# Optimization experiments

Hardware: AMD Instinct MI355X
Metric: run time of the kernel (lower is better)

Reference implementation:

```python
import jax, jax.numpy as jnp
import numpy as np

N, E, H, RBF, NZ = 15000, 300000, 128, 20, 119
CUTOFF, BOX = 6.0, 7.0


def setup_inputs() -> dict:
    key = jax.random.key(0)
    ks = jax.random.split(key, 24)
    s = 0.05

    def rn(k, shape):
        return jax.random.normal(k, shape, dtype=jnp.float32) * s

    z = jax.random.randint(ks[0], (N,), 0, 83)
    pos = jax.random.uniform(ks[1], (N, 3), dtype=jnp.float32) * BOX
    src = jax.random.randint(ks[2], (E,), 0, N)
    dst = (src + jax.random.randint(ks[3], (E,), 1, N)) % N  # guarantees src != dst
    edge_index = jnp.stack([src, dst], axis=0)  # (2, E)
    cell_offsets = (jax.random.randint(ks[4], (E, 3), 0, 3) - 1).astype(jnp.float32)
    cell = jnp.eye(3, dtype=jnp.float32) * BOX
    return dict(
        z=z, pos=pos, edge_index=edge_index, cell_offsets=cell_offsets, cell=cell,
        embed=rn(ks[5], (NZ, H)),
        msg_w1=rn(ks[6], (3, H, H)), msg_b1=rn(ks[7], (3, H)),
        msg_w2=rn(ks[8], (3, H, 3 * H)), msg_b2=rn(ks[9], (3, 3 * H)),
        filt_w=rn(ks[10], (3, RBF, 3 * H)), filt_b=rn(ks[11], (3, 3 * H)),
        upd_uw=rn(ks[12], (3, H, H)), upd_ub=rn(ks[13], (3, H)),
        upd_vw=rn(ks[14], (3, H, H)), upd_vb=rn(ks[15], (3, H)),
        upd_mw1=rn(ks[16], (3, 2 * H, H)), upd_mb1=rn(ks[17], (3, H)),
        upd_mw2=rn(ks[18], (3, H, 3 * H)), upd_mb2=rn(ks[19], (3, 3 * H)),
        head_w1=rn(ks[20], (H, H)), head_b1=rn(ks[21], (H,)),
        head_w2=rn(ks[22], (H, H)), head_b2=rn(ks[23], (H,)),
    )


def reference(z, pos, edge_index, cell_offsets, cell, embed,
              msg_w1, msg_b1, msg_w2, msg_b2, filt_w, filt_b,
              upd_uw, upd_ub, upd_vw, upd_vb,
              upd_mw1, upd_mb1, upd_mw2, upd_mb2,
              head_w1, head_b1, head_w2, head_b2):
    n_nodes = z.shape[0]
    hdim = embed.shape[1]
    row, col = edge_index[0], edge_index[1]  # receiver, sender (DeepDFT convention)

    # get_pbc_distances
    offsets = cell_offsets @ cell                                  # (E,3)
    edge_diff = pos[row] - pos[col] + offsets                      # (E,3)
    edge_dist = jnp.linalg.norm(edge_diff, axis=-1)                # (E,)
    unit = edge_diff / edge_dist[:, None]                          # (E,3)

    # sinc radial basis + cosine cutoff (shared by all message layers)
    n = jnp.arange(1, RBF + 1, dtype=pos.dtype)
    rbf = jnp.sin(edge_dist[:, None] * n * jnp.pi / CUTOFF) / edge_dist[:, None]  # (E,RBF)
    fcut = jnp.where(edge_dist < CUTOFF,
                     0.5 * (jnp.cos(jnp.pi * edge_dist / CUTOFF) + 1.0), 0.0)      # (E,)

    ns = embed[z]                                                  # (N,H)
    nv = jnp.zeros((n_nodes, 3, hdim), dtype=pos.dtype)            # (N,3,H)

    for i in range(3):
        # ---- PainnMessage ----
        filt = (rbf @ filt_w[i] + filt_b[i]) * fcut[:, None]       # (E,3H)
        sout = jax.nn.silu(ns @ msg_w1[i] + msg_b1[i]) @ msg_w2[i] + msg_b2[i]  # (N,3H)
        fo = filt * sout[col]                                      # (E,3H)
        gate_v, gate_e, msg_s = jnp.split(fo, 3, axis=1)           # each (E,H)
        msg_v = nv[col] * gate_v[:, None, :] + gate_e[:, None, :] * unit[:, :, None]  # (E,3,H)
        ns = ns + jax.ops.segment_sum(msg_s, row, num_segments=n_nodes)
        nv = nv + jax.ops.segment_sum(msg_v, row, num_segments=n_nodes)
        # ---- PainnUpdate ----
        Uv = nv @ upd_uw[i] + upd_ub[i]                            # (N,3,H)
        Vv = nv @ upd_vw[i] + upd_vb[i]                            # (N,3,H)
        mlp_in = jnp.concatenate([jnp.linalg.norm(Vv, axis=1), ns], axis=1)  # (N,2H)
        m = jax.nn.silu(mlp_in @ upd_mw1[i] + upd_mb1[i]) @ upd_mw2[i] + upd_mb2[i]  # (N,3H)
        a_vv, a_sv, a_ss = jnp.split(m, 3, axis=1)
        inner = jnp.sum(Uv * Vv, axis=1)                           # (N,H)
        nv = nv + a_vv[:, None, :] * Uv
        ns = ns + a_sv * inner + a_ss

    v = jax.nn.silu(ns @ head_w1 + head_b1) @ head_w2 + head_b2    # (N,H)
    return v, edge_dist
```

## Files before the change

### kernel.cpp

```cpp
#include <hip/hip_runtime.h>
#include <math.h>

#define HD 128
#define H3 384
#define RBF_N 20
#define CUTOFF_R 6.0f
#define PI_F 3.14159265358979323846f
#define CAPE 40000

#define PITCH 136

typedef __attribute__((ext_vector_type(8))) short short8v;
typedef __attribute__((ext_vector_type(4))) short short4v;
typedef __attribute__((ext_vector_type(4))) float f32x4;
typedef unsigned short bf_t;

__device__ __forceinline__ float silu_f(float x) { return x / (1.0f + __expf(-x)); }

__device__ __forceinline__ ushort f2bf(float f) {
    union { float f; uint u; } v; v.f = f;
    return (ushort)((v.u + 0x7FFF + ((v.u >> 16) & 1)) >> 16);
}
__device__ __forceinline__ float bf2f(ushort x) {
    union { uint u; float f; } v; v.u = ((uint)x) << 16;
    return v.f;
}

#define LOADWG(r, CNT, NTH, W, rowlen, koff)                                   \
    _Pragma("unroll")                                                          \
    for (int it_ = 0; it_ < CNT; ++it_) {                                      \
        int u_ = tid + it_ * NTH;                                              \
        (r)[it_] = *(const short8v*)((W) + (size_t)(u_ >> 4) * (rowlen) +      \
                                     (koff) + ((u_ & 15) << 3));               \
    }
#define COMMITB(r, CNT, NTH, WT)                                               \
    _Pragma("unroll")                                                          \
    for (int it_ = 0; it_ < CNT; ++it_) {                                      \
        int u_ = tid + it_ * NTH;                                              \
        *(short8v*)&WT[(u_ >> 4) * PITCH + ((u_ & 15) << 3)] = (r)[it_];       \
    }
#define MFMA8B(Abuf, acc, WT)                                                  \
    _Pragma("unroll")                                                          \
    for (int step_ = 0; step_ < 4; ++step_) {                                  \
        int kb_ = step_ * 32 + lk;                                             \
        short8v a_ = *(const short8v*)&(Abuf)[(wr + lr) * PITCH + kb_];        \
        (acc)[0] = __builtin_amdgcn_mfma_f32_16x16x32_bf16(                    \
            a_, *(const short8v*)&WT[(wn + lr) * PITCH + kb_], (acc)[0], 0, 0, 0); \
        (acc)[1] = __builtin_amdgcn_mfma_f32_16x16x32_bf16(                    \
            a_, *(const short8v*)&WT[(wn + 16 + lr) * PITCH + kb_], (acc)[1], 0, 0, 0); \
    }
#define MFMA8R(Abuf, acc)                                                      \
    _Pragma("unroll")                                                          \
    for (int step_ = 0; step_ < 4; ++step_) {                                  \
        int kb_ = step_ * 32 + lk;                                             \
        short8v a_ = *(const short8v*)&(Abuf)[(wr + lr) * PITCH + kb_];        \
        (acc)[0] = __builtin_amdgcn_mfma_f32_16x16x32_bf16(                    \
            a_, *(const short8v*)&Wt[(wn + lr) * PITCH + kb_], (acc)[0], 0, 0, 0); \
        (acc)[1] = __builtin_amdgcn_mfma_f32_16x16x32_bf16(                    \
            a_, *(const short8v*)&Wt[(wn + 16 + lr) * PITCH + kb_], (acc)[1], 0, 0, 0); \
    }
#define COMMITWG(r, CNT, NTH)                                                  \
    _Pragma("unroll")                                                          \
    for (int it_ = 0; it_ < CNT; ++it_) {                                      \
        int u_ = tid + it_ * NTH;                                              \
        *(short8v*)&Wt[(u_ >> 4) * PITCH + ((u_ & 15) << 3)] = (r)[it_];       \
    }

__device__ __forceinline__ void wcvt(const float* __restrict__ src, bf_t* __restrict__ dst,
                                     int idx, int K, int N) {
    int per = K * N;
    int l = idx / per, r = idx % per;
    int k = r / N, n = r % N;
    dst[(size_t)l*per + (size_t)n*K + k] = f2bf(src[(size_t)l*per + (size_t)k*N + n]);
}

__global__ void setup1_kernel(const float* __restrict__ pos, const int* __restrict__ ei,
                              const float* __restrict__ cofs, const float* __restrict__ cell,
                              float* __restrict__ dist_out, int* __restrict__ deg, int E, int eb,
                              const float* s0, const float* s1, const float* s2, const float* s3,
                              const float* s4, const float* s5, const float* s6, const float* s7,
                              const float* s8, bf_t* __restrict__ dst) {
    if ((int)blockIdx.x < eb) {
        int e = blockIdx.x * 256 + threadIdx.x;
        if (e >= E) return;
        int r = ei[e], c = ei[E + e];
        float c0 = cofs[3*e], c1 = cofs[3*e+1], c2 = cofs[3*e+2];
        float d0 = pos[3*r]   - pos[3*c]   + c0*cell[0] + c1*cell[3] + c2*cell[6];
        float d1 = pos[3*r+1] - pos[3*c+1] + c0*cell[1] + c1*cell[4] + c2*cell[7];
        float d2 = pos[3*r+2] - pos[3*c+2] + c0*cell[2] + c1*cell[5] + c2*cell[8];
        float dist = sqrtf(d0*d0 + d1*d1 + d2*d2);
        dist_out[e] = dist;
        if (dist < CUTOFF_R) atomicAdd(&deg[r], 1);
    } else {
        int i = (blockIdx.x - eb) * 256 + threadIdx.x;
        if (i < 49152)        wcvt(s0, dst + 0,      i - 0,      128, 128);
        else if (i < 196608)  wcvt(s1, dst + 49152,  i - 49152,  128, 384);
        else if (i < 245760)  wcvt(s2, dst + 196608, i - 196608, 128, 128);
        else if (i < 294912)  wcvt(s3, dst + 245760, i - 245760, 128, 128);
        else if (i < 393216)  wcvt(s4, dst + 294912, i - 294912, 256, 128);
        else if (i < 540672)  wcvt(s5, dst + 393216, i - 393216, 128, 384);
        else if (i < 557056)  wcvt(s6, dst + 540672, i - 540672, 128, 128);
        else if (i < 573440)  wcvt(s7, dst + 557056, i - 557056, 128, 128);
        else if (i < 596480)  dst[i] = f2bf(s8[i - 573440]);
    }
}

__global__ void scan_kernel(const int* __restrict__ deg, int* __restrict__ off,
                            int* __restrict__ cursor, int n) {
    __shared__ int wsum[16];
    __shared__ int carry_s;
    const int tid = threadIdx.x;
    const int lane = tid & 63, wv = tid >> 6;
    if (tid == 0) carry_s = 0;
    __syncthreads();
    for (int base = 0; base < n; base += 1024) {
        int v = (base + tid < n) ? deg[base + tid] : 0;
        int x = v;
        #pragma unroll
        for (int s = 1; s < 64; s <<= 1) {
            int y = __shfl_up(x, s);
            if (lane >= s) x += y;
        }
        if (lane == 63) wsum[wv] = x;
        __syncthreads();
        if (tid == 0) {
            int a = carry_s;
            #pragma unroll
            for (int i = 0; i < 16; ++i) { int t = wsum[i]; wsum[i] = a; a += t; }
            carry_s = a;
        }
        __syncthreads();
        int exc = wsum[wv] + x - v;
        if (base + tid < n) { off[base + tid] = exc; cursor[base + tid] = exc; }
        __syncthreads();
    }
    if (tid == 0) off[n] = carry_s;
}

__global__ __launch_bounds__(512) void setup2_kernel(
        const float* __restrict__ pos, const int* __restrict__ ei,
        const float* __restrict__ cofs, const float* __restrict__ cell,
        const float* __restrict__ dist_in, int* __restrict__ cursor,
        int* __restrict__ col_s, float* __restrict__ fcut_s,
        float* __restrict__ unit_s, float* __restrict__ rbf_s, int E, int sb,
        const int* __restrict__ z, const float* __restrict__ emb,
        bf_t* __restrict__ nsb,
        const bf_t* __restrict__ W1b, const float* __restrict__ b1,
        const bf_t* __restrict__ W2b, const float* __restrict__ b2,
        bf_t* __restrict__ Cb, int M) {
    __shared__ ushort As[32 * PITCH];
    __shared__ ushort Wt[128 * PITCH];
    __shared__ ushort Hid[32 * PITCH];
    const int tid = threadIdx.x;

    if ((int)blockIdx.x < sb) {
        int e = blockIdx.x * 512 + tid;
        if (e >= E) return;
        float dist = dist_in[e];
        if (!(dist < CUTOFF_R)) return;
        int r = ei[e], c = ei[E + e];
        float c0 = cofs[3*e], c1 = cofs[3*e+1], c2 = cofs[3*e+2];
        float d0 = pos[3*r]   - pos[3*c]   + c0*cell[0] + c1*cell[3] + c2*cell[6];
        float d1 = pos[3*r+1] - pos[3*c+1] + c0*cell[1] + c1*cell[4] + c2*cell[7];
        float d2 = pos[3*r+2] - pos[3*c+2] + c0*cell[2] + c1*cell[5] + c2*cell[8];
        int p = atomicAdd(&cursor[r], 1);
        if (p >= CAPE) return;
        col_s[p] = c;
        fcut_s[p] = 0.5f * (cosf(PI_F * dist / CUTOFF_R) + 1.0f);
        float inv = 1.0f / dist;
        unit_s[3*p]   = d0 * inv;
        unit_s[3*p+1] = d1 * inv;
        unit_s[3*p+2] = d2 * inv;
        #pragma unroll
        for (int j = 0; j < RBF_N; ++j)
            rbf_s[(size_t)p*RBF_N + j] = sinf(dist * (float)(j+1) * (PI_F / CUTOFF_R)) * inv;
        return;
    }

    const int m0 = (blockIdx.x - sb) * 32;
    const int wid = tid >> 6, lane = tid & 63;
    const int wr = (wid >> 2) * 16;
    const int wn = (wid & 3) * 32;
    const int lr = lane & 15, lk = (lane >> 4) << 3;
    const int er = (lane >> 4) << 2;

    short8v rwA[4], rwB[4];
    LOADWG(rwA, 4, 512, W1b, 128, 0);
    {
        int row = tid >> 4, k8 = (tid & 15) << 3;
        int m = m0 + row;
        short8v pk = (short8v)(0);
        if (m < M) {
            const float* ep = emb + (size_t)z[m] * HD + k8;
            const float4 x = *(const float4*)ep, y = *(const float4*)(ep + 4);
            pk[0]=(short)f2bf(x.x); pk[1]=(short)f2bf(x.y);
            pk[2]=(short)f2bf(x.z); pk[3]=(short)f2bf(x.w);
            pk[4]=(short)f2bf(y.x); pk[5]=(short)f2bf(y.y);
            pk[6]=(short)f2bf(y.z); pk[7]=(short)f2bf(y.w);
            *(short8v*)(nsb + (size_t)m * HD + k8) = pk;
        }
        *(short8v*)&As[row * PITCH + k8] = pk;
    }
    __syncthreads();
    COMMITWG(rwA, 4, 512); LOADWG(rwB, 4, 512, W2b, 128, 0);
    __syncthreads();
    f32x4 acc1[2];
    acc1[0] = (f32x4)(0.f); acc1[1] = (f32x4)(0.f);
    MFMA8R(As, acc1);
    __syncthreads();
    COMMITWG(rwB, 4, 512); LOADWG(rwA, 4, 512, W2b + 16384, 128, 0);
    #pragma unroll
    for (int j = 0; j < 2; ++j) {
        int col = wn + 16 * j + lr;
        float bb = b1[col];
        #pragma unroll
        for (int r = 0; r < 4; ++r)
            Hid[(wr + er + r) * PITCH + col] = f2bf(silu_f(acc1[j][r] + bb));
    }
    __syncthreads();
    {
        f32x4 a0[2]; a0[0] = (f32x4)(0.f); a0[1] = (f32x4)(0.f);
        MFMA8R(Hid, a0);
        __syncthreads();
        COMMITWG(rwA, 4, 512); LOADWG(rwB, 4, 512, W2b + 32768, 128, 0);
        #pragma unroll
        for (int j = 0; j < 2; ++j) {
            int col = wn + 16 * j + lr;
            float bb = b2[col];
            #pragma unroll
            for (int r = 0; r < 4; ++r) {
                int m = m0 + wr + er + r;
                if (m < M) Cb[(size_t)m * H3 + col] = f2bf(a0[j][r] + bb);
            }
        }
        __syncthreads();
    }
    {
        f32x4 a1[2]; a1[0] = (f32x4)(0.f); a1[1] = (f32x4)(0.f);
        MFMA8R(Hid, a1);
        __syncthreads();
        COMMITWG(rwB, 4, 512);
        #pragma unroll
        for (int j = 0; j < 2; ++j) {
            int col = wn + 16 * j + lr;
            float bb = b2[128 + col];
            #pragma unroll
            for (int r = 0; r < 4; ++r) {
                int m = m0 + wr + er + r;
                if (m < M) Cb[(size_t)m * H3 + 128 + col] = f2bf(a1[j][r] + bb);
            }
        }
        __syncthreads();
    }
    {
        f32x4 a2[2]; a2[0] = (f32x4)(0.f); a2[1] = (f32x4)(0.f);
        MFMA8R(Hid, a2);
        #pragma unroll
        for (int j = 0; j < 2; ++j) {
            int col = wn + 16 * j + lr;
            float bb = b2[256 + col];
            #pragma unroll
            for (int r = 0; r < 4; ++r) {
                int m = m0 + wr + er + r;
                if (m < M) Cb[(size_t)m * H3 + 256 + col] = f2bf(a2[j][r] + bb);
            }
        }
    }
}

template <int MODE>
__global__ __launch_bounds__(1024) void upd_fused(const bf_t* __restrict__ nv2p,
                                                 const bf_t* __restrict__ Ub,
                                                 const bf_t* __restrict__ Vb,
                                                 const float* __restrict__ bu,
                                                 const float* __restrict__ bv,
                                                 bf_t* __restrict__ nvp,
                                                 bf_t* __restrict__ nsb,
                                                 const bf_t* __restrict__ W1b,
                                                 const float* __restrict__ b1,
                                                 const bf_t* __restrict__ W2b,
                                                 const float* __restrict__ b2,
                                                 const bf_t* __restrict__ xw1,
                                                 const float* __restrict__ xb1,
                                                 const bf_t* __restrict__ xw2,
                                                 const float* __restrict__ xb2,
                                                 bf_t* __restrict__ soutb,
                                                 float* __restrict__ Cf,
                                                 int N) {
    __shared__ ushort As3[3][64 * PITCH];
    __shared__ ushort Wt0[128 * PITCH];
    __shared__ ushort Wt1[128 * PITCH];
    __shared__ ushort Hid[64 * PITCH];
    __shared__ ushort AsG[64 * PITCH];
    const int tid = threadIdx.x;
    const int m0 = blockIdx.x * 64;
    const int wid = tid >> 6, lane = tid & 63;
    const int wr = (wid >> 2) * 16;
    const int wn = (wid & 3) * 32;
    const int lr = lane & 15, lk = (lane >> 4) << 3;
    const int er = (lane >> 4) << 2;
    const size_t NHD = (size_t)N * HD;

    short8v rwA[2], rwB[2];
    LOADWG(rwA, 2, 1024, Ub, 128, 0);

    #pragma unroll
    for (int it = 0; it < 3; ++it) {
        int u = tid + it * 1024;
        int d = u >> 10, v = u & 1023;
        int row = v >> 4, k8 = (v & 15) << 3;
        int m = m0 + row;
        short8v pk = (short8v)(0);
        if (m < N) pk = *(const short8v*)(nv2p + (size_t)d * NHD + (size_t)m * HD + k8);
        *(short8v*)&As3[d][row * PITCH + k8] = pk;
    }
    {
        int row = tid >> 4, k8 = (tid & 15) << 3;
        int m = m0 + row;
        short8v pk = (short8v)(0);
        if (m < N) pk = *(const short8v*)(nsb + (size_t)m * HD + k8);
        *(short8v*)&AsG[row * PITCH + k8] = pk;
    }
    __syncthreads();
    COMMITB(rwA, 2, 1024, Wt0); LOADWG(rwB, 2, 1024, Vb, 128, 0);
    __syncthreads();

    f32x4 aU[3][2], aV[3][2];
    #pragma unroll
    for (int d = 0; d < 3; ++d) {
        aU[d][0] = (f32x4)(0.f); aU[d][1] = (f32x4)(0.f);
        aV[d][0] = (f32x4)(0.f); aV[d][1] = (f32x4)(0.f);
    }
    #pragma unroll
    for (int d = 0; d < 3; ++d) { MFMA8B(As3[d], aU[d], Wt0); }
    COMMITB(rwB, 2, 1024, Wt1); LOADWG(rwA, 2, 1024, W1b, 256, 0);
    __syncthreads();

    #pragma unroll
    for (int d = 0; d < 3; ++d) { MFMA8B(As3[d], aV[d], Wt1); }
    float inn_r[2][4];
    #pragma unroll
    for (int j = 0; j < 2; ++j) {
        int col = wn + 16 * j + lr;
        float bbu = bu[col], bbv = bv[col];
        #pragma unroll
        for (int r = 0; r < 4; ++r) {
            float inn = 0.f, nrm = 0.f;
            #pragma unroll
            for (int d = 0; d < 3; ++d) {
                float u = aU[d][j][r] + bbu;
                float v = aV[d][j][r] + bbv;
                aU[d][j][r] = u;
                inn += u * v;
                nrm += v * v;
            }
            inn_r[j][r] = inn;
            Hid[(wr + er + r) * PITCH + col] = f2bf(sqrtf(nrm));
        }
    }
    COMMITB(rwA, 2, 1024, Wt0); LOADWG(rwB, 2, 1024, W1b, 256, 128);
    __syncthreads();

    f32x4 acc1[2]; acc1[0] = (f32x4)(0.f); acc1[1] = (f32x4)(0.f);
    MFMA8B(Hid, acc1, Wt0);
    COMMITB(rwB, 2, 1024, Wt1);
    if (MODE == 1) { LOADWG(rwA, 2, 1024, W2b, 128, 0); }
    else           { LOADWG(rwA, 2, 1024, W2b + 16384, 128, 0); }
    __syncthreads();

    MFMA8B(AsG, acc1, Wt1);
    #pragma unroll
    for (int j = 0; j < 2; ++j) {
        int col = wn + 16 * j + lr;
        float bb = b1[col];
        #pragma unroll
        for (int r = 0; r < 4; ++r)
            Hid[(wr + er + r) * PITCH + col] = f2bf(silu_f(acc1[j][r] + bb));
    }
    COMMITB(rwA, 2, 1024, Wt0);
    if (MODE == 1) { LOADWG(rwB, 2, 1024, W2b + 16384, 128, 0); }
    else           { LOADWG(rwB, 2, 1024, W2b + 32768, 128, 0); }
    __syncthreads();

    float sv[2][4];
    if (MODE == 1) {
        f32x4 g0[2]; g0[0] = (f32x4)(0.f); g0[1] = (f32x4)(0.f);
        MFMA8B(Hid, g0, Wt0);
        #pragma unroll
        for (int j = 0; j < 2; ++j) {
            int col = wn + 16 * j + lr;
            float bb = b2[col];
            #pragma unroll
            for (int r = 0; r < 4; ++r) {
                int m = m0 + wr + er + r;
                if (m < N) {
                    float g = g0[j][r] + bb;
                    #pragma unroll
                    for (int d = 0; d < 3; ++d) {
                        float pp = bf2f(As3[d][(wr + er + r) * PITCH + col]);
                        nvp[(size_t)d * NHD + (size_t)m * HD + col] =
                            f2bf(pp + g * aU[d][j][r]);
                    }
                }
            }
        }
        COMMITB(rwB, 2, 1024, Wt1); LOADWG(rwA, 2, 1024, W2b + 32768, 128, 0);
        __syncthreads();
        f32x4 g1[2]; g1[0] = (f32x4)(0.f); g1[1] = (f32x4)(0.f);
        MFMA8B(Hid, g1, Wt1);
        #pragma unroll
        for (int j = 0; j < 2; ++j) {
            int col = wn + 16 * j + lr;
            float bb = b2[128 + col];
            #pragma unroll
            for (int r = 0; r < 4; ++r)
                sv[j][r] = (g1[j][r] + bb) * inn_r[j][r];
        }
        COMMITB(rwA, 2, 1024, Wt0); LOADWG(rwB, 2, 1024, xw1, 128, 0);
        __syncthreads();
        f32x4 g2[2]; g2[0] = (f32x4)(0.f); g2[1] = (f32x4)(0.f);
        MFMA8B(Hid, g2, Wt0);
        #pragma unroll
        for (int j = 0; j < 2; ++j) {
            int col = wn + 16 * j + lr;
            float bb = b2[256 + col];
            #pragma unroll
            for (int r = 0; r < 4; ++r) {
                int m = m0 + wr + er + r;
                if (m < N) {
                    int idx = (wr + er + r) * PITCH + col;
                    float s = bf2f(AsG[idx]) + sv[j][r] + (g2[j][r] + bb);
                    ushort sb = f2bf(s);
                    AsG[idx] = sb;
                    nsb[(size_t)m * HD + col] = sb;
                }
            }
        }
        COMMITB(rwB, 2, 1024, Wt1); LOADWG(rwA, 2, 1024, xw2, 128, 0);
        __syncthreads();
        f32x4 ah[2]; ah[0] = (f32x4)(0.f); ah[1] = (f32x4)(0.f);
        MFMA8B(AsG, ah, Wt1);
        #pragma unroll
        for (int j = 0; j < 2; ++j) {
            int col = wn + 16 * j + lr;
            float bb = xb1[col];
            #pragma unroll
            for (int r = 0; r < 4; ++r)
                Hid[(wr + er + r) * PITCH + col] = f2bf(silu_f(ah[j][r] + bb));
        }
        COMMITB(rwA, 2, 1024, Wt0); LOADWG(rwB, 2, 1024, xw2 + 16384, 128, 0);
        __syncthreads();
        {
            f32x4 o0[2]; o0[0] = (f32x4)(0.f); o0[1] = (f32x4)(0.f);
            MFMA8B(Hid, o0, Wt0);
            #pragma unroll
            for (int j = 0; j < 2; ++j) {
                int col = wn + 16 * j + lr;
                float bb = xb2[col];
                #pragma unroll
                for (int r = 0; r < 4; ++r) {
                    int m = m0 + wr + er + r;
                    if (m < N) soutb[(size_t)m * H3 + col] = f2bf(o0[j][r] + bb);
                }
            }
        }
        COMMITB(rwB, 2, 1024, Wt1); LOADWG(rwA, 2, 1024, xw2 + 32768, 128, 0);
        __syncthreads();
        {
            f32x4 o1[2]; o1[0] = (f32x4)(0.f); o1[1] = (f32x4)(0.f);
            MFMA8B(Hid, o1, Wt1);
            #pragma unroll
            for (int j = 0; j < 2; ++j) {
                int col = wn + 16 * j + lr;
                float bb = xb2[128 + col];
                #pragma unroll
                for (int r = 0; r < 4; ++r) {
                    int m = m0 + wr + er + r;
                    if (m < N) soutb[(size_t)m * H3 + 128 + col] = f2bf(o1[j][r] + bb);
                }
            }
        }
        COMMITB(rwA, 2, 1024, Wt0);
        __syncthreads();
        {
            f32x4 o2[2]; o2[0] = (f32x4)(0.f); o2[1] = (f32x4)(0.f);
            MFMA8B(Hid, o2, Wt0);
            #pragma unroll
            for (int j = 0; j < 2; ++j) {
                int col = wn + 16 * j + lr;
                float bb = xb2[256 + col];
                #pragma unroll
                for (int r = 0; r < 4; ++r) {
                    int m = m0 + wr + er + r;
                    if (m < N) soutb[(size_t)m * H3 + 256 + col] = f2bf(o2[j][r] + bb);
                }
            }
        }
    } else {
        f32x4 g1[2]; g1[0] = (f32x4)(0.f); g1[1] = (f32x4)(0.f);
        MFMA8B(Hid, g1, Wt0);
        #pragma unroll
        for (int j = 0; j < 2; ++j) {
            int col = wn + 16 * j + lr;
            float bb = b2[128 + col];
            #pragma unroll
            for (int r = 0; r < 4; ++r)
                sv[j][r] = (g1[j][r] + bb) * inn_r[j][r];
        }
        COMMITB(rwB, 2, 1024, Wt1); LOADWG(rwA, 2, 1024, xw1, 128, 0);
        __syncthreads();
        f32x4 g2[2]; g2[0] = (f32x4)(0.f); g2[1] = (f32x4)(0.f);
        MFMA8B(Hid, g2, Wt1);
        #pragma unroll
        for (int j = 0; j < 2; ++j) {
            int col = wn + 16 * j + lr;
            float bb = b2[256 + col];
            #pragma unroll
            for (int r = 0; r < 4; ++r) {
                int idx = (wr + er + r) * PITCH + col;
                float s = bf2f(AsG[idx]) + sv[j][r] + (g2[j][r] + bb);
                AsG[idx] = f2bf(s);
            }
        }
        COMMITB(rwA, 2, 1024, Wt0); LOADWG(rwB, 2, 1024, xw2, 128, 0);
        __syncthreads();
        f32x4 ah[2]; ah[0] = (f32x4)(0.f); ah[1] = (f32x4)(0.f);
        MFMA8B(AsG, ah, Wt0);
        #pragma unroll
        for (int j = 0; j < 2; ++j) {
            int col = wn + 16 * j + lr;
            float bb = xb1[col];
            #pragma unroll
            for (int r = 0; r < 4; ++r)
                Hid[(wr + er + r) * PITCH + col] = f2bf(silu_f(ah[j][r] + bb));
        }
        COMMITB(rwB, 2, 1024, Wt1);
        __syncthreads();
        f32x4 ao[2]; ao[0] = (f32x4)(0.f); ao[1] = (f32x4)(0.f);
        MFMA8B(Hid, ao, Wt1);
        #pragma unroll
        for (int j = 0; j < 2; ++j) {
            int col = wn + 16 * j + lr;
            float bb = xb2[col];
            #pragma unroll
            for (int r = 0; r < 4; ++r) {
                int m = m0 + wr + er + r;
                if (m < N) Cf[(size_t)m * HD + col] = ao[j][r] + bb;
            }
        }
    }
}

template <int FIRST>
__global__ __launch_bounds__(128) void message_kernel(
        bf_t* __restrict__ ns_b,
        const bf_t* __restrict__ nv_b, bf_t* __restrict__ nv2_b,
        const bf_t* __restrict__ sout,
        const int* __restrict__ col_s, const float* __restrict__ unit_s,
        const float* __restrict__ rbf_s, const float* __restrict__ fcut_s,
        const bf_t* __restrict__ Wf_b, const float* __restrict__ bf_g,
        const int* __restrict__ off, int n_nodes) {
    const int t = threadIdx.x;
    const int nA = blockIdx.x * 2;
    if (nA >= n_nodes) return;
    const int nB = nA + 1;
    const bool hasB = (nB < n_nodes);
    const size_t NHD = (size_t)n_nodes * HD;

    float w0[RBF_N], w1[RBF_N], w2[RBF_N];
    #pragma unroll
    for (int r = 0; r < RBF_N; ++r) {
        w0[r] = bf2f(Wf_b[r * H3 + t]);
        w1[r] = bf2f(Wf_b[r * H3 + HD + t]);
        w2[r] = bf2f(Wf_b[r * H3 + 2*HD + t]);
    }
    const float bb0 = bf_g[t], bb1 = bf_g[HD + t], bb2 = bf_g[2*HD + t];

    int e0   = off[nA];
    int endA = off[nA + 1];
    int end  = hasB ? off[nB + 1] : endA;
    if (endA > CAPE) endA = CAPE;
    if (end  > CAPE) end  = CAPE;

    float aS = 0.f, a0 = 0.f, a1 = 0.f, a2 = 0.f;
    float bS = 0.f, b0 = 0.f, b1 = 0.f, b2 = 0.f;

    int e = e0;
    for (; e + 1 < end; e += 2) {
        int cX = col_s[e], cY = col_s[e + 1];
        float fcX = fcut_s[e], fcY = fcut_s[e + 1];
        float uX0 = unit_s[3*e],   uX1 = unit_s[3*e+1], uX2 = unit_s[3*e+2];
        float uY0 = unit_s[3*e+3], uY1 = unit_s[3*e+4], uY2 = unit_s[3*e+5];
        float fX0 = bb0, fX1 = bb1, fX2 = bb2;
        float fY0 = bb0, fY1 = bb1, fY2 = bb2;
        const float* rbX = rbf_s + (size_t)e * RBF_N;
        const float* rbY = rbX + RBF_N;
        #pragma unroll
        for (int r = 0; r < RBF_N; ++r) {
            float rx = rbX[r], ry = rbY[r];
            fX0 += rx * w0[r]; fY0 += ry * w0[r];
            fX1 += rx * w1[r]; fY1 += ry * w1[r];
            fX2 += rx * w2[r]; fY2 += ry * w2[r];
        }
        const bf_t* spX = sout + (size_t)cX * H3;
        const bf_t* spY = sout + (size_t)cY * H3;
        float gvX = fX0 * fcX * bf2f(spX[t]);
        float geX = fX1 * fcX * bf2f(spX[HD+t]);
        float msX = fX2 * fcX * bf2f(spX[2*HD+t]);
        float gvY = fY0 * fcY * bf2f(spY[t]);
        float geY = fY1 * fcY * bf2f(spY[HD+t]);
        float msY = fY2 * fcY * bf2f(spY[2*HD+t]);
        float vX0, vX1, vX2, vY0, vY1, vY2;
        if (FIRST) {
            vX0 = geX * uX0; vX1 = geX * uX1; vX2 = geX * uX2;
            vY0 = geY * uY0; vY1 = geY * uY1; vY2 = geY * uY2;
        } else {
            const bf_t* nvX = nv_b + (size_t)cX * HD + t;
            const bf_t* nvY = nv_b + (size_t)cY * HD + t;
            vX0 = bf2f(nvX[0])     * gvX + geX * uX0;
            vX1 = bf2f(nvX[NHD])   * gvX + geX * uX1;
            vX2 = bf2f(nvX[2*NHD]) * gvX + geX * uX2;
            vY0 = bf2f(nvY[0])     * gvY + geY * uY0;
            vY1 = bf2f(nvY[NHD])   * gvY + geY * uY1;
            vY2 = bf2f(nvY[2*NHD]) * gvY + geY * uY2;
        }
        if (e < endA) { a0 += vX0; a1 += vX1; a2 += vX2; aS += msX; }
        else          { b0 += vX0; b1 += vX1; b2 += vX2; bS += msX; }
        if (e + 1 < endA) { a0 += vY0; a1 += vY1; a2 += vY2; aS += msY; }
        else              { b0 += vY0; b1 += vY1; b2 += vY2; bS += msY; }
    }
    if (e < end) {
        int c = col_s[e];
        float fc = fcut_s[e];
        float u0 = unit_s[3*e], u1 = unit_s[3*e+1], u2 = unit_s[3*e+2];
        float f0 = bb0, f1 = bb1, f2 = bb2;
        const float* rb = rbf_s + (size_t)e * RBF_N;
        #pragma unroll
        for (int r = 0; r < RBF_N; ++r) {
            float rv = rb[r];
            f0 += rv * w0[r];
            f1 += rv * w1[r];
            f2 += rv * w2[r];
        }
        const bf_t* sp = sout + (size_t)c * H3;
        float gv = f0 * fc * bf2f(sp[t]);
        float ge = f1 * fc * bf2f(sp[HD+t]);
        float ms = f2 * fc * bf2f(sp[2*HD+t]);
        float v0, v1, v2;
        if (FIRST) {
            v0 = ge * u0; v1 = ge * u1; v2 = ge * u2;
        } else {
            const bf_t* nvc = nv_b + (size_t)c * HD + t;
            v0 = bf2f(nvc[0])     * gv + ge * u0;
            v1 = bf2f(nvc[NHD])   * gv + ge * u1;
            v2 = bf2f(nvc[2*NHD]) * gv + ge * u2;
        }
        if (e < endA) { a0 += v0; a1 += v1; a2 += v2; aS += ms; }
        else          { b0 += v0; b1 += v1; b2 += v2; bS += ms; }
    }

    {
        size_t b = (size_t)nA * HD + t;
        if (FIRST) {
            nv2_b[b]         = f2bf(a0);
            nv2_b[b + NHD]   = f2bf(a1);
            nv2_b[b + 2*NHD] = f2bf(a2);
        } else {
            nv2_b[b]         = f2bf(bf2f(nv_b[b])         + a0);
            nv2_b[b + NHD]   = f2bf(bf2f(nv_b[b + NHD])   + a1);
            nv2_b[b + 2*NHD] = f2bf(bf2f(nv_b[b + 2*NHD]) + a2);
        }
        if (endA > e0) {
            size_t so = (size_t)nA * HD + t;
            ns_b[so] = f2bf(bf2f(ns_b[so]) + aS);
        }
    }
    if (hasB) {
        size_t b = (size_t)nB * HD + t;
        if (FIRST) {
            nv2_b[b]         = f2bf(b0);
            nv2_b[b + NHD]   = f2bf(b1);
            nv2_b[b + 2*NHD] = f2bf(b2);
        } else {
            nv2_b[b]         = f2bf(bf2f(nv_b[b])         + b0);
            nv2_b[b + NHD]   = f2bf(bf2f(nv_b[b + NHD])   + b1);
            nv2_b[b + 2*NHD] = f2bf(bf2f(nv_b[b + 2*NHD]) + b2);
        }
        if (end > endA) {
            size_t so = (size_t)nB * HD + t;
            ns_b[so] = f2bf(bf2f(ns_b[so]) + bS);
        }
    }
}

extern "C" void kernel_launch(void* const* d_in, const int* in_sizes, int n_in,
                              void* d_out, int out_size, void* d_ws, size_t ws_size,
                              hipStream_t stream) {
    const int*   z       = (const int*)  d_in[0];
    const float* pos     = (const float*)d_in[1];
    const int*   ei      = (const int*)  d_in[2];
    const float* cofs    = (const float*)d_in[3];
    const float* cell    = (const float*)d_in[4];
    const float* emb     = (const float*)d_in[5];
    const float* msg_w1  = (const float*)d_in[6];
    const float* msg_b1  = (const float*)d_in[7];
    const float* msg_w2  = (const float*)d_in[8];
    const float* msg_b2  = (const float*)d_in[9];
    const float* filt_w  = (const float*)d_in[10];
    const float* filt_b  = (const float*)d_in[11];
    const float* upd_uw  = (const float*)d_in[12];
    const float* upd_ub  = (const float*)d_in[13];
    const float* upd_vw  = (const float*)d_in[14];
    const float* upd_vb  = (const float*)d_in[15];
    const float* upd_mw1 = (const float*)d_in[16];
    const float* upd_mb1 = (const float*)d_in[17];
    const float* upd_mw2 = (const float*)d_in[18];
    const float* upd_mb2 = (const float*)d_in[19];
    const float* head_w1 = (const float*)d_in[20];
    const float* head_b1 = (const float*)d_in[21];
    const float* head_w2 = (const float*)d_in[22];
    const float* head_b2 = (const float*)d_in[23];

    const int N = in_sizes[0];
    const int E = in_sizes[2] / 2;

    float* out_v    = (float*)d_out;
    float* out_dist = out_v + (size_t)N * HD;

    char* p = (char*)d_ws;
    auto alloc = [&](size_t bytes) -> void* {
        void* r = (void*)p;
        p += (bytes + 255) & ~(size_t)255;
        return r;
    };
    bf_t*  ns_b   = (bf_t*) alloc((size_t)N * HD * 2);
    bf_t*  nv_b   = (bf_t*) alloc((size_t)N * H3 * 2);
    bf_t*  nv2_b  = (bf_t*) alloc((size_t)N * H3 * 2);
    bf_t*  sout   = (bf_t*) alloc((size_t)N * H3 * 2);
    bf_t*  wb     = (bf_t*) alloc((size_t)596480 * 2);
    float* rbf_s  = (float*)alloc((size_t)CAPE * RBF_N * 4);
    float* fcut_s = (float*)alloc((size_t)CAPE * 4);
    float* unit_s = (float*)alloc((size_t)CAPE * 3 * 4);
    int*   col_s  = (int*)  alloc((size_t)CAPE * 4);
    int*   deg    = (int*)  alloc((size_t)N * 4);
    int*   off    = (int*)  alloc((size_t)(N + 1) * 4);
    int*   cursor = (int*)  alloc((size_t)N * 4);

    hipMemsetAsync(deg, 0, (size_t)N * 4, stream);

    const bf_t* w_msg1 = wb + 0;
    const bf_t* w_msg2 = wb + 49152;
    const bf_t* w_uw   = wb + 196608;
    const bf_t* w_vw   = wb + 245760;
    const bf_t* w_mw1  = wb + 294912;
    const bf_t* w_mw2  = wb + 393216;
    const bf_t* w_hw1  = wb + 540672;
    const bf_t* w_hw2  = wb + 557056;
    const bf_t* w_fw   = wb + 573440;

    int eb = (E + 255) / 256;
    int wpb = (596480 + 255) / 256;
    setup1_kernel<<<eb + wpb, 256, 0, stream>>>(
        pos, ei, cofs, cell, out_dist, deg, E, eb,
        msg_w1, msg_w2, upd_uw, upd_vw, upd_mw1, upd_mw2, head_w1, head_w2, filt_w, wb);
    scan_kernel<<<1, 1024, 0, stream>>>(deg, off, cursor, N);
    int sb = (E + 511) / 512;
    int mt32 = (N + 31) / 32;
    setup2_kernel<<<sb + mt32, 512, 0, stream>>>(
        pos, ei, cofs, cell, out_dist, cursor,
        col_s, fcut_s, unit_s, rbf_s, E, sb,
        z, emb, ns_b, w_msg1, msg_b1, w_msg2, msg_b2, sout, N);

    int mt64 = (N + 63) / 64;
    int mpairs = (N + 1) / 2;
    for (int i = 0; i < 3; ++i) {
        if (i == 0)
            message_kernel<1><<<mpairs, 128, 0, stream>>>(
                ns_b, nv_b, nv2_b, sout, col_s, unit_s, rbf_s, fcut_s,
                w_fw + (size_t)i*RBF_N*H3, filt_b + (size_t)i*H3, off, N);
        else
            message_kernel<0><<<mpairs, 128, 0, stream>>>(
                ns_b, nv_b, nv2_b, sout, col_s, unit_s, rbf_s, fcut_s,
                w_fw + (size_t)i*RBF_N*H3, filt_b + (size_t)i*H3, off, N);
        if (i < 2) {
            upd_fused<1><<<mt64, 1024, 0, stream>>>(
                nv2_b, w_uw + (size_t)i*16384, w_vw + (size_t)i*16384,
                upd_ub + (size_t)i*HD, upd_vb + (size_t)i*HD,
                nv_b, ns_b,
                w_mw1 + (size_t)i*32768, upd_mb1 + (size_t)i*HD,
                w_mw2 + (size_t)i*49152, upd_mb2 + (size_t)i*H3,
                w_msg1 + (size_t)(i+1)*16384, msg_b1 + (size_t)(i+1)*HD,
                w_msg2 + (size_t)(i+1)*49152, msg_b2 + (size_t)(i+1)*H3,
                sout, nullptr, N);
        } else {
            upd_fused<3><<<mt64, 1024, 0, stream>>>(
                nv2_b, w_uw + (size_t)i*16384, w_vw + (size_t)i*16384,
                upd_ub + (size_t)i*HD, upd_vb + (size_t)i*HD,
                nv_b, ns_b,
                w_mw1 + (size_t)i*32768, upd_mb1 + (size_t)i*HD,
                w_mw2 + (size_t)i*49152, upd_mb2 + (size_t)i*H3,
                w_hw1, head_b1, w_hw2, head_b2,
                nullptr, out_v, N);
        }
    }
}
```

Measured before the change: 198.2 us.

## Fuse edge message aggregation into the node update kernel with ping-pong buffers

```diff
diff --git a/kernel.cpp b/kernel.cpp
--- a/kernel.cpp
+++ b/kernel.cpp
@@ -11,7 +11,6 @@
 #define PITCH 136
 
 typedef __attribute__((ext_vector_type(8))) short short8v;
-typedef __attribute__((ext_vector_type(4))) short short4v;
 typedef __attribute__((ext_vector_type(4))) float f32x4;
 typedef unsigned short bf_t;
 
@@ -268,25 +267,21 @@
     }
 }
 
-template <int MODE>
-__global__ __launch_bounds__(1024) void upd_fused(const bf_t* __restrict__ nv2p,
-                                                 const bf_t* __restrict__ Ub,
-                                                 const bf_t* __restrict__ Vb,
-                                                 const float* __restrict__ bu,
-                                                 const float* __restrict__ bv,
-                                                 bf_t* __restrict__ nvp,
-                                                 bf_t* __restrict__ nsb,
-                                                 const bf_t* __restrict__ W1b,
-                                                 const float* __restrict__ b1,
-                                                 const bf_t* __restrict__ W2b,
-                                                 const float* __restrict__ b2,
-                                                 const bf_t* __restrict__ xw1,
-                                                 const float* __restrict__ xb1,
-                                                 const bf_t* __restrict__ xw2,
-                                                 const float* __restrict__ xb2,
-                                                 bf_t* __restrict__ soutb,
-                                                 float* __restrict__ Cf,
-                                                 int N) {
+template <int MODE, int FIRST>
+__global__ __launch_bounds__(1024) void upd_fused(
+        const bf_t* __restrict__ sout_in, const bf_t* __restrict__ nv_in,
+        const int* __restrict__ col_s, const float* __restrict__ unit_s,
+        const float* __restrict__ rbf_s, const float* __restrict__ fcut_s,
+        const int* __restrict__ off,
+        const bf_t* __restrict__ Wf_b, const float* __restrict__ bf_g,
+        const bf_t* __restrict__ Ub, const bf_t* __restrict__ Vb,
+        const float* __restrict__ bu, const float* __restrict__ bv,
+        bf_t* __restrict__ nvp, bf_t* __restrict__ nsb,
+        const bf_t* __restrict__ W1b, const float* __restrict__ b1,
+        const bf_t* __restrict__ W2b, const float* __restrict__ b2,
+        const bf_t* __restrict__ xw1, const float* __restrict__ xb1,
+        const bf_t* __restrict__ xw2, const float* __restrict__ xb2,
+        bf_t* __restrict__ soutb, float* __restrict__ Cf, int N) {
     __shared__ ushort As3[3][64 * PITCH];
     __shared__ ushort Wt0[128 * PITCH];
     __shared__ ushort Wt1[128 * PITCH];
@@ -304,22 +299,67 @@
     short8v rwA[2], rwB[2];
     LOADWG(rwA, 2, 1024, Ub, 128, 0);
 
-    #pragma unroll
-    for (int it = 0; it < 3; ++it) {
-        int u = tid + it * 1024;
-        int d = u >> 10, v = u & 1023;
-        int row = v >> 4, k8 = (v & 15) << 3;
-        int m = m0 + row;
-        short8v pk = (short8v)(0);
-        if (m < N) pk = *(const short8v*)(nv2p + (size_t)d * NHD + (size_t)m * HD + k8);
-        *(short8v*)&As3[d][row * PITCH + k8] = pk;
-    }
     {
-        int row = tid >> 4, k8 = (tid & 15) << 3;
-        int m = m0 + row;
-        short8v pk = (short8v)(0);
-        if (m < N) pk = *(const short8v*)(nsb + (size_t)m * HD + k8);
-        *(short8v*)&AsG[row * PITCH + k8] = pk;
+        const int sub = tid >> 7;
+        const int chan = tid & 127;
+        float w0r[RBF_N], w1r[RBF_N], w2r[RBF_N];
+        #pragma unroll
+        for (int r = 0; r < RBF_N; ++r) {
+            w0r[r] = bf2f(Wf_b[r * H3 + chan]);
+            w1r[r] = bf2f(Wf_b[r * H3 + HD + chan]);
+            w2r[r] = bf2f(Wf_b[r * H3 + 2*HD + chan]);
+        }
+        const float bb0 = bf_g[chan], bb1 = bf_g[HD + chan], bb2 = bf_g[2*HD + chan];
+        for (int ng = 0; ng < 8; ++ng) {
+            int row = ng * 8 + sub;
+            int node = m0 + row;
+            ushort s0v = 0, s1v = 0, s2v = 0, sgv = 0;
+            if (node < N) {
+                float aS = 0.f, a0 = 0.f, a1 = 0.f, a2 = 0.f;
+                int e0 = off[node], e1 = off[node + 1];
+                if (e1 > CAPE) e1 = CAPE;
+                for (int e = e0; e < e1; ++e) {
+                    int c = col_s[e];
+                    float fc = fcut_s[e];
+                    const float* rb = rbf_s + (size_t)e * RBF_N;
+                    float f0 = bb0, f1 = bb1, f2 = bb2;
+                    #pragma unroll
+                    for (int r = 0; r < RBF_N; ++r) {
+                        float rv = rb[r];
+                        f0 += rv * w0r[r];
+                        f1 += rv * w1r[r];
+                        f2 += rv * w2r[r];
+                    }
+                    const bf_t* sp = sout_in + (size_t)c * H3;
+                    float gv = f0 * fc * bf2f(sp[chan]);
+                    float ge = f1 * fc * bf2f(sp[HD + chan]);
+                    float ms = f2 * fc * bf2f(sp[2*HD + chan]);
+                    float u0 = unit_s[3*e], u1 = unit_s[3*e+1], u2 = unit_s[3*e+2];
+                    if (FIRST) {
+                        a0 += ge * u0; a1 += ge * u1; a2 += ge * u2;
+                    } else {
+                        const bf_t* nvc = nv_in + (size_t)c * HD + chan;
+                        a0 += bf2f(nvc[0])     * gv + ge * u0;
+                        a1 += bf2f(nvc[NHD])   * gv + ge * u1;
+                        a2 += bf2f(nvc[2*NHD]) * gv + ge * u2;
+                    }
+                    aS += ms;
+                }
+                size_t b = (size_t)node * HD + chan;
+                if (FIRST) {
+                    s0v = f2bf(a0); s1v = f2bf(a1); s2v = f2bf(a2);
+                } else {
+                    s0v = f2bf(bf2f(nv_in[b])         + a0);
+                    s1v = f2bf(bf2f(nv_in[b + NHD])   + a1);
+                    s2v = f2bf(bf2f(nv_in[b + 2*NHD]) + a2);
+                }
+                sgv = f2bf(bf2f(nsb[b]) + aS);
+            }
+            As3[0][row * PITCH + chan] = s0v;
+            As3[1][row * PITCH + chan] = s1v;
+            As3[2][row * PITCH + chan] = s2v;
+            AsG[row * PITCH + chan]    = sgv;
+        }
     }
     __syncthreads();
     COMMITB(rwA, 2, 1024, Wt0); LOADWG(rwB, 2, 1024, Vb, 128, 0);
@@ -547,148 +587,6 @@
                 int m = m0 + wr + er + r;
                 if (m < N) Cf[(size_t)m * HD + col] = ao[j][r] + bb;
             }
-        }
-    }
-}
-
-template <int FIRST>
-__global__ __launch_bounds__(128) void message_kernel(
-        bf_t* __restrict__ ns_b,
-        const bf_t* __restrict__ nv_b, bf_t* __restrict__ nv2_b,
-        const bf_t* __restrict__ sout,
-        const int* __restrict__ col_s, const float* __restrict__ unit_s,
-        const float* __restrict__ rbf_s, const float* __restrict__ fcut_s,
-        const bf_t* __restrict__ Wf_b, const float* __restrict__ bf_g,
-        const int* __restrict__ off, int n_nodes) {
-    const int t = threadIdx.x;
-    const int nA = blockIdx.x * 2;
-    if (nA >= n_nodes) return;
-    const int nB = nA + 1;
-    const bool hasB = (nB < n_nodes);
-    const size_t NHD = (size_t)n_nodes * HD;
-
-    float w0[RBF_N], w1[RBF_N], w2[RBF_N];
-    #pragma unroll
-    for (int r = 0; r < RBF_N; ++r) {
-        w0[r] = bf2f(Wf_b[r * H3 + t]);
-        w1[r] = bf2f(Wf_b[r * H3 + HD + t]);
-        w2[r] = bf2f(Wf_b[r * H3 + 2*HD + t]);
-    }
-    const float bb0 = bf_g[t], bb1 = bf_g[HD + t], bb2 = bf_g[2*HD + t];
-
-    int e0   = off[nA];
-    int endA = off[nA + 1];
-    int end  = hasB ? off[nB + 1] : endA;
-    if (endA > CAPE) endA = CAPE;
-    if (end  > CAPE) end  = CAPE;
-
-    float aS = 0.f, a0 = 0.f, a1 = 0.f, a2 = 0.f;
-    float bS = 0.f, b0 = 0.f, b1 = 0.f, b2 = 0.f;
-
-    int e = e0;
-    for (; e + 1 < end; e += 2) {
-        int cX = col_s[e], cY = col_s[e + 1];
-        float fcX = fcut_s[e], fcY = fcut_s[e + 1];
-        float uX0 = unit_s[3*e],   uX1 = unit_s[3*e+1], uX2 = unit_s[3*e+2];
-        float uY0 = unit_s[3*e+3], uY1 = unit_s[3*e+4], uY2 = unit_s[3*e+5];
-        float fX0 = bb0, fX1 = bb1, fX2 = bb2;
-        float fY0 = bb0, fY1 = bb1, fY2 = bb2;
-        const float* rbX = rbf_s + (size_t)e * RBF_N;
-        const float* rbY = rbX + RBF_N;
-        #pragma unroll
-        for (int r = 0; r < RBF_N; ++r) {
-            float rx = rbX[r], ry = rbY[r];
-            fX0 += rx * w0[r]; fY0 += ry * w0[r];
-            fX1 += rx * w1[r]; fY1 += ry * w1[r];
-            fX2 += rx * w2[r]; fY2 += ry * w2[r];
-        }
-        const bf_t* spX = sout + (size_t)cX * H3;
-        const bf_t* spY = sout + (size_t)cY * H3;
-        float gvX = fX0 * fcX * bf2f(spX[t]);
-        float geX = fX1 * fcX * bf2f(spX[HD+t]);
-        float msX = fX2 * fcX * bf2f(spX[2*HD+t]);
-        float gvY = fY0 * fcY * bf2f(spY[t]);
-        float geY = fY1 * fcY * bf2f(spY[HD+t]);
-        float msY = fY2 * fcY * bf2f(spY[2*HD+t]);
-        float vX0, vX1, vX2, vY0, vY1, vY2;
-        if (FIRST) {
-            vX0 = geX * uX0; vX1 = geX * uX1; vX2 = geX * uX2;
-            vY0 = geY * uY0; vY1 = geY * uY1; vY2 = geY * uY2;
-        } else {
-            const bf_t* nvX = nv_b + (size_t)cX * HD + t;
-            const bf_t* nvY = nv_b + (size_t)cY * HD + t;
-            vX0 = bf2f(nvX[0])     * gvX + geX * uX0;
-            vX1 = bf2f(nvX[NHD])   * gvX + geX * uX1;
-            vX2 = bf2f(nvX[2*NHD]) * gvX + geX * uX2;
-            vY0 = bf2f(nvY[0])     * gvY + geY * uY0;
-            vY1 = bf2f(nvY[NHD])   * gvY + geY * uY1;
-            vY2 = bf2f(nvY[2*NHD]) * gvY + geY * uY2;
-        }
-        if (e < endA) { a0 += vX0; a1 += vX1; a2 += vX2; aS += msX; }
-        else          { b0 += vX0; b1 += vX1; b2 += vX2; bS += msX; }
-        if (e + 1 < endA) { a0 += vY0; a1 += vY1; a2 += vY2; aS += msY; }
-        else              { b0 += vY0; b1 += vY1; b2 += vY2; bS += msY; }
-    }
-    if (e < end) {
-        int c = col_s[e];
-        float fc = fcut_s[e];
-        float u0 = unit_s[3*e], u1 = unit_s[3*e+1], u2 = unit_s[3*e+2];
-        float f0 = bb0, f1 = bb1, f2 = bb2;
-        const float* rb = rbf_s + (size_t)e * RBF_N;
-        #pragma unroll
-        for (int r = 0; r < RBF_N; ++r) {
-            float rv = rb[r];
-            f0 += rv * w0[r];
-            f1 += rv * w1[r];
-            f2 += rv * w2[r];
-        }
-        const bf_t* sp = sout + (size_t)c * H3;
-        float gv = f0 * fc * bf2f(sp[t]);
-        float ge = f1 * fc * bf2f(sp[HD+t]);
-        float ms = f2 * fc * bf2f(sp[2*HD+t]);
-        float v0, v1, v2;
-        if (FIRST) {
-            v0 = ge * u0; v1 = ge * u1; v2 = ge * u2;
-        } else {
-            const bf_t* nvc = nv_b + (size_t)c * HD + t;
-            v0 = bf2f(nvc[0])     * gv + ge * u0;
-            v1 = bf2f(nvc[NHD])   * gv + ge * u1;
-            v2 = bf2f(nvc[2*NHD]) * gv + ge * u2;
-        }
-        if (e < endA) { a0 += v0; a1 += v1; a2 += v2; aS += ms; }
-        else          { b0 += v0; b1 += v1; b2 += v2; bS += ms; }
-    }
-
-    {
-        size_t b = (size_t)nA * HD + t;
-        if (FIRST) {
-            nv2_b[b]         = f2bf(a0);
-            nv2_b[b + NHD]   = f2bf(a1);
-            nv2_b[b + 2*NHD] = f2bf(a2);
-        } else {
-            nv2_b[b]         = f2bf(bf2f(nv_b[b])         + a0);
-            nv2_b[b + NHD]   = f2bf(bf2f(nv_b[b + NHD])   + a1);
-            nv2_b[b + 2*NHD] = f2bf(bf2f(nv_b[b + 2*NHD]) + a2);
-        }
-        if (endA > e0) {
-            size_t so = (size_t)nA * HD + t;
-            ns_b[so] = f2bf(bf2f(ns_b[so]) + aS);
-        }
-    }
-    if (hasB) {
-        size_t b = (size_t)nB * HD + t;
-        if (FIRST) {
-            nv2_b[b]         = f2bf(b0);
-            nv2_b[b + NHD]   = f2bf(b1);
-            nv2_b[b + 2*NHD] = f2bf(b2);
-        } else {
-            nv2_b[b]         = f2bf(bf2f(nv_b[b])         + b0);
-            nv2_b[b + NHD]   = f2bf(bf2f(nv_b[b + NHD])   + b1);
-            nv2_b[b + 2*NHD] = f2bf(bf2f(nv_b[b + 2*NHD]) + b2);
-        }
-        if (end > endA) {
-            size_t so = (size_t)nB * HD + t;
-            ns_b[so] = f2bf(bf2f(ns_b[so]) + bS);
         }
     }
 }
@@ -734,9 +632,10 @@
         return r;
     };
     bf_t*  ns_b   = (bf_t*) alloc((size_t)N * HD * 2);
-    bf_t*  nv_b   = (bf_t*) alloc((size_t)N * H3 * 2);
-    bf_t*  nv2_b  = (bf_t*) alloc((size_t)N * H3 * 2);
-    bf_t*  sout   = (bf_t*) alloc((size_t)N * H3 * 2);
+    bf_t*  nvA    = (bf_t*) alloc((size_t)N * H3 * 2);
+    bf_t*  nvB    = (bf_t*) alloc((size_t)N * H3 * 2);
+    bf_t*  soutA  = (bf_t*) alloc((size_t)N * H3 * 2);
+    bf_t*  soutB  = (bf_t*) alloc((size_t)N * H3 * 2);
     bf_t*  wb     = (bf_t*) alloc((size_t)596480 * 2);
     float* rbf_s  = (float*)alloc((size_t)CAPE * RBF_N * 4);
     float* fcut_s = (float*)alloc((size_t)CAPE * 4);
@@ -769,38 +668,37 @@
     setup2_kernel<<<sb + mt32, 512, 0, stream>>>(
         pos, ei, cofs, cell, out_dist, cursor,
         col_s, fcut_s, unit_s, rbf_s, E, sb,
-        z, emb, ns_b, w_msg1, msg_b1, w_msg2, msg_b2, sout, N);
+        z, emb, ns_b, w_msg1, msg_b1, w_msg2, msg_b2, soutA, N);
 
     int mt64 = (N + 63) / 64;
-    int mpairs = (N + 1) / 2;
-    for (int i = 0; i < 3; ++i) {
-        if (i == 0)
-            message_kernel<1><<<mpairs, 128, 0, stream>>>(
-                ns_b, nv_b, nv2_b, sout, col_s, unit_s, rbf_s, fcut_s,
-                w_fw + (size_t)i*RBF_N*H3, filt_b + (size_t)i*H3, off, N);
-        else
-            message_kernel<0><<<mpairs, 128, 0, stream>>>(
-                ns_b, nv_b, nv2_b, sout, col_s, unit_s, rbf_s, fcut_s,
-                w_fw + (size_t)i*RBF_N*H3, filt_b + (size_t)i*H3, off, N);
-        if (i < 2) {
-            upd_fused<1><<<mt64, 1024, 0, stream>>>(
-                nv2_b, w_uw + (size_t)i*16384, w_vw + (size_t)i*16384,
-                upd_ub + (size_t)i*HD, upd_vb + (size_t)i*HD,
-                nv_b, ns_b,
-                w_mw1 + (size_t)i*32768, upd_mb1 + (size_t)i*HD,
-                w_mw2 + (size_t)i*49152, upd_mb2 + (size_t)i*H3,
-                w_msg1 + (size_t)(i+1)*16384, msg_b1 + (size_t)(i+1)*HD,
-                w_msg2 + (size_t)(i+1)*49152, msg_b2 + (size_t)(i+1)*H3,
-                sout, nullptr, N);
-        } else {
-            upd_fused<3><<<mt64, 1024, 0, stream>>>(
-                nv2_b, w_uw + (size_t)i*16384, w_vw + (size_t)i*16384,
-                upd_ub + (size_t)i*HD, upd_vb + (size_t)i*HD,
-                nv_b, ns_b,
-                w_mw1 + (size_t)i*32768, upd_mb1 + (size_t)i*HD,
-                w_mw2 + (size_t)i*49152, upd_mb2 + (size_t)i*H3,
-                w_hw1, head_b1, w_hw2, head_b2,
-                nullptr, out_v, N);
-        }
-    }
+    upd_fused<1, 1><<<mt64, 1024, 0, stream>>>(
+        soutA, nvA, col_s, unit_s, rbf_s, fcut_s, off,
+        w_fw + 0, filt_b + 0,
+        w_uw + 0, w_vw + 0, upd_ub + 0, upd_vb + 0,
+        nvB, ns_b,
+        w_mw1 + 0, upd_mb1 + 0, w_mw2 + 0, upd_mb2 + 0,
+        w_msg1 + (size_t)1*16384, msg_b1 + (size_t)1*HD,
+        w_msg2 + (size_t)1*49152, msg_b2 + (size_t)1*H3,
+        soutB, nullptr, N);
+    upd_fused<1, 0><<<mt64, 1024, 0, stream>>>(
+        soutB, nvB, col_s, unit_s, rbf_s, fcut_s, off,
+        w_fw + (size_t)1*RBF_N*H3, filt_b + (size_t)1*H3,
+        w_uw + (size_t)1*16384, w_vw + (size_t)1*16384,
+        upd_ub + (size_t)1*HD, upd_vb + (size_t)1*HD,
+        nvA, ns_b,
+        w_mw1 + (size_t)1*32768, upd_mb1 + (size_t)1*HD,
+        w_mw2 + (size_t)1*49152, upd_mb2 + (size_t)1*H3,
+        w_msg1 + (size_t)2*16384, msg_b1 + (size_t)2*HD,
+        w_msg2 + (size_t)2*49152, msg_b2 + (size_t)2*H3,
+        soutA, nullptr, N);
+    upd_fused<3, 0><<<mt64, 1024, 0, stream>>>(
+        soutA, nvA, col_s, unit_s, rbf_s, fcut_s, off,
+        w_fw + (size_t)2*RBF_N*H3, filt_b + (size_t)2*H3,
+        w_uw + (size_t)2*16384, w_vw + (size_t)2*16384,
+        upd_ub + (size_t)2*HD, upd_vb + (size_t)2*HD,
+        nvB, ns_b,
+        w_mw1 + (size_t)2*32768, upd_mb1 + (size_t)2*HD,
+        w_mw2 + (size_t)2*49152, upd_mb2 + (size_t)2*H3,
+        w_hw1, head_b1, w_hw2, head_b2,
+        nullptr, out_v, N);
 }
```

Measured after the change: 257.7 us. 1.3x slower.
